# Optimization experiments

Measured on AMD Instinct MI355X. Metric: run time of the kernel, lower is better.

The kernel has to match this reference:

```python
import jax, jax.numpy as jnp
import numpy as np

IN_FEATURES = 4096
OUT_FEATURES = 4096
Q_MAX = 127.0  # int8 activation range
EPS = 1e-10


def setup_inputs() -> dict:
    key = jax.random.key(0)
    k1, k2, k3 = jax.random.split(key, 3)
    x = jax.random.normal(k1, (4, 2048, IN_FEATURES), dtype=jnp.float32)
    # Ternary weight in {-1, 0, +1} (the unpacked content of w_packed from pack_tl1).
    w_raw = jax.random.normal(k2, (OUT_FEATURES, IN_FEATURES), dtype=jnp.float32)
    scale = jnp.mean(jnp.abs(w_raw))  # quantize_ternary: scale = |w|.mean()
    w_t = jnp.clip(jnp.round(w_raw / (scale + EPS)), -1.0, 1.0)
    bias = jax.random.normal(k3, (OUT_FEATURES,), dtype=jnp.float32)
    return {"x": x, "w_t": w_t, "w_scale": scale, "bias": bias}


def reference(x, w_t, w_scale, bias):
    """TernaryLinear forward: per-row int8 activation quant, ternary matmul
    with int32 accumulation, scale dequant, bias add.

    x: [..., in], w_t: [out, in] in {-1,0,+1}, w_scale: scalar, bias: [out].
    """
    lead = x.shape[:-1]
    x2 = x.reshape(-1, IN_FEATURES)  # [T, in]
    # Per-row absmax int8 quantization of activations.
    absmax = jnp.max(jnp.abs(x2), axis=-1, keepdims=True)  # [T, 1]
    act_scale = jnp.maximum(absmax, EPS) / Q_MAX
    xq = jnp.clip(jnp.round(x2 / act_scale), -Q_MAX, Q_MAX)  # int-valued [T, in]
    # int32 accumulation (exact in int32; values bounded by 127 * 4096).
    acc = jnp.matmul(xq.astype(jnp.int32), w_t.astype(jnp.int32).T)  # [T, out]
    # Dequantize: y ~= (x @ w_t.T) * w_scale, then bias.
    y = acc.astype(jnp.float32) * act_scale * w_scale + bias
    return y.reshape(*lead, OUT_FEATURES)
```

## Files before the change

### kernel.cpp

```cpp
#include <hip/hip_runtime.h>
#include <stdint.h>

#define T_ROWS 8192
#define IN_F 4096
#define OUT_F 4096

using i32x4 = __attribute__((ext_vector_type(4))) int;

#define GLOBAL_AS __attribute__((address_space(1)))
#define LDS_AS __attribute__((address_space(3)))

static __device__ __forceinline__ void load_lds16(const void* g, void* l) {
    __builtin_amdgcn_global_load_lds((const GLOBAL_AS uint32_t*)g,
                                     (LDS_AS uint32_t*)l, 16, 0, 0);
}

__global__ __launch_bounds__(256) void prep_kernel(const float* __restrict__ x,
                                                   int8_t* __restrict__ xq,
                                                   float* __restrict__ scales,
                                                   const float* __restrict__ w,
                                                   int8_t* __restrict__ w8) {
    if (blockIdx.x < T_ROWS) {
        const int row = blockIdx.x;
        const float* xr = x + (size_t)row * IN_F;
        const float4* xr4 = (const float4*)xr;

        float4 v[4];
        float amax = 0.0f;
#pragma unroll
        for (int i = 0; i < 4; ++i) {
            v[i] = xr4[threadIdx.x + 256 * i];
            amax = fmaxf(amax, fmaxf(fmaxf(fabsf(v[i].x), fabsf(v[i].y)),
                                     fmaxf(fabsf(v[i].z), fabsf(v[i].w))));
        }
#pragma unroll
        for (int off = 32; off; off >>= 1)
            amax = fmaxf(amax, __shfl_xor(amax, off, 64));
        __shared__ float smax[4];
        if ((threadIdx.x & 63) == 0) smax[threadIdx.x >> 6] = amax;
        __syncthreads();
        amax = fmaxf(fmaxf(smax[0], smax[1]), fmaxf(smax[2], smax[3]));

        const float act_scale = fmaxf(amax, 1e-10f) / 127.0f;
        if (threadIdx.x == 0) scales[row] = act_scale;

        int* xqr = (int*)(xq + (size_t)row * IN_F);
#pragma unroll
        for (int i = 0; i < 4; ++i) {
            int q0 = (int)fminf(fmaxf(rintf(v[i].x / act_scale), -127.0f), 127.0f);
            int q1 = (int)fminf(fmaxf(rintf(v[i].y / act_scale), -127.0f), 127.0f);
            int q2 = (int)fminf(fmaxf(rintf(v[i].z / act_scale), -127.0f), 127.0f);
            int q3 = (int)fminf(fmaxf(rintf(v[i].w / act_scale), -127.0f), 127.0f);
            int packed = (q0 & 0xff) | ((q1 & 0xff) << 8) | ((q2 & 0xff) << 16) | (q3 << 24);
            xqr[threadIdx.x + 256 * i] = packed;
        }
    } else {
        const float4* w4 = (const float4*)w;
        int* o4 = (int*)w8;
        size_t base = (size_t)(blockIdx.x - T_ROWS) * 1024 + threadIdx.x;
#pragma unroll
        for (int i = 0; i < 4; ++i) {
            size_t idx = base + 256 * i;
            float4 v = w4[idx];
            int q0 = (int)v.x, q1 = (int)v.y, q2 = (int)v.z, q3 = (int)v.w;
            o4[idx] = (q0 & 0xff) | ((q1 & 0xff) << 8) | ((q2 & 0xff) << 16) | (q3 << 24);
        }
    }
}

__global__ __launch_bounds__(512, 2) void gemm_kernel(const int8_t* __restrict__ xq,
                                                      const int8_t* __restrict__ w8,
                                                      const float* __restrict__ scales,
                                                      const float* __restrict__ bias,
                                                      const float* __restrict__ wscale_p,
                                                      float* __restrict__ out) {
    __shared__ __align__(16) int8_t As[2 * 256 * 128];
    __shared__ __align__(16) int8_t Bs[2 * 256 * 128];

    const int tid = threadIdx.x;
    const int lane = tid & 63;
    const int w = tid >> 6;
    const int wr = w >> 2;
    const int wc = w & 3;
    const int l16 = lane & 15;
    const int lq = lane >> 4;

    int bid = blockIdx.x;
    bid = (bid & 7) * 64 + (bid >> 3);
    const int brow = (bid >> 4) * 256;
    const int bcol = (bid & 15) * 256;

    const int lrow = lane >> 3;
    const int lslot = (lane & 7) ^ lrow;
    const int8_t* srcA = xq + (size_t)(brow + lrow) * IN_F + lslot * 16;
    const int8_t* srcB = w8 + (size_t)(bcol + lrow) * IN_F + lslot * 16;

    const int sA = l16 & 7;
    const int8_t* pA0 = As + (wr * 16 + l16) * 128 + ((lq ^ sA) << 4);
    const int8_t* pA1 = As + (wr * 16 + l16) * 128 + (((lq ^ sA) ^ 4) << 4);
    const int8_t* pB0 = Bs + (wc * 16 + l16) * 128 + ((lq ^ sA) << 4);
    const int8_t* pB1 = Bs + (wc * 16 + l16) * 128 + (((lq ^ sA) ^ 4) << 4);

#define STAGE(LDSA, SRC, BUF, H, KT) do {                                          \
    load_lds16((SRC) + (size_t)((H) * 128 + w * 8) * IN_F + (KT) * 128,            \
               (void*)((LDSA) + (BUF) * 32768 + ((H) * 16 + w) * 1024));           \
    load_lds16((SRC) + (size_t)((H) * 128 + (w + 8) * 8) * IN_F + (KT) * 128,      \
               (void*)((LDSA) + (BUF) * 32768 + ((H) * 16 + w + 8) * 1024));       \
} while (0)

#define READ_A(BUF, MH)                                                            \
    _Pragma("unroll") for (int m = 0; m < 4; ++m) {                                \
        ra[m][0] = *(const i32x4*)(pA0 + (BUF) * 32768 + ((MH) * 4 + m) * 4096);   \
        ra[m][1] = *(const i32x4*)(pA1 + (BUF) * 32768 + ((MH) * 4 + m) * 4096);   \
    }

#define READ_B(BUF, NH, RB)                                                        \
    _Pragma("unroll") for (int n = 0; n < 2; ++n) {                                \
        RB[n][0] = *(const i32x4*)(pB0 + (BUF) * 32768 + ((NH) * 2 + n) * 8192);   \
        RB[n][1] = *(const i32x4*)(pB1 + (BUF) * 32768 + ((NH) * 2 + n) * 8192);   \
    }

#define PHASE(READS, STAGE_STMT, MH, NH, RB, VM_STMT) do {                         \
    READS;                                                                         \
    STAGE_STMT;                                                                    \
    __builtin_amdgcn_s_setprio(1);                                                 \
    _Pragma("unroll") for (int m = 0; m < 4; ++m)                                  \
    _Pragma("unroll") for (int n = 0; n < 2; ++n) {                                \
        acc[(MH) * 4 + m][(NH) * 2 + n] = __builtin_amdgcn_mfma_i32_16x16x64_i8(   \
            ra[m][0], RB[n][0], acc[(MH) * 4 + m][(NH) * 2 + n], 0, 0, 0);         \
        acc[(MH) * 4 + m][(NH) * 2 + n] = __builtin_amdgcn_mfma_i32_16x16x64_i8(   \
            ra[m][1], RB[n][1], acc[(MH) * 4 + m][(NH) * 2 + n], 0, 0, 0);         \
    }                                                                              \
    __builtin_amdgcn_s_setprio(0);                                                 \
    VM_STMT;                                                                       \
    __builtin_amdgcn_s_barrier();                                                  \
    asm volatile("" ::: "memory");                                                 \
} while (0)

    i32x4 acc[8][4] = {};
    i32x4 ra[4][2], rb0[2][2], rb1[2][2];

    STAGE(As, srcA, 0, 0, 0);
    STAGE(Bs, srcB, 0, 0, 0);
    STAGE(Bs, srcB, 0, 1, 0);
    STAGE(As, srcA, 0, 1, 0);
    STAGE(As, srcA, 1, 0, 1);
    STAGE(Bs, srcB, 1, 0, 1);
    STAGE(Bs, srcB, 1, 1, 1);
    asm volatile("s_waitcnt vmcnt(6)" ::: "memory");
    __builtin_amdgcn_s_barrier();
    asm volatile("" ::: "memory");

    for (int t = 0; t < 16; ++t) {
        const int k1 = 2 * t + 1;
        const int k2 = (2 * t + 2) & 31;
        const int k3 = (2 * t + 3) & 31;
        PHASE(READ_B(0, 0, rb0); READ_A(0, 0), STAGE(As, srcA, 1, 1, k1), 0, 0, rb0, );
        PHASE(READ_B(0, 1, rb1),               STAGE(As, srcA, 0, 0, k2), 0, 1, rb1, );
        PHASE(READ_A(0, 1),                    STAGE(Bs, srcB, 0, 0, k2), 1, 1, rb1, );
        PHASE(,                                STAGE(Bs, srcB, 0, 1, k2), 1, 0, rb0,
              asm volatile("s_waitcnt vmcnt(6)" ::: "memory"));
        PHASE(READ_B(1, 0, rb0); READ_A(1, 0), STAGE(As, srcA, 0, 1, k2), 0, 0, rb0, );
        PHASE(READ_B(1, 1, rb1),               STAGE(As, srcA, 1, 0, k3), 0, 1, rb1, );
        PHASE(READ_A(1, 1),                    STAGE(Bs, srcB, 1, 0, k3), 1, 1, rb1, );
        PHASE(,                                STAGE(Bs, srcB, 1, 1, k3), 1, 0, rb0,
              asm volatile("s_waitcnt vmcnt(6)" ::: "memory"));
    }

    const float ws = wscale_p[0];
#pragma unroll
    for (int m = 0; m < 8; ++m) {
        const int row0 = brow + m * 32 + wr * 16 + lq * 4;
#pragma unroll
        for (int j = 0; j < 4; ++j) {
            const int row = row0 + j;
            const float sc = scales[row] * ws;
#pragma unroll
            for (int n = 0; n < 4; ++n) {
                const int col = bcol + n * 64 + wc * 16 + l16;
                out[(size_t)row * OUT_F + col] = (float)acc[m][n][j] * sc + bias[col];
            }
        }
    }
#undef STAGE
#undef READ_A
#undef READ_B
#undef PHASE
}

extern "C" void kernel_launch(void* const* d_in, const int* in_sizes, int n_in,
                              void* d_out, int out_size, void* d_ws, size_t ws_size,
                              hipStream_t stream) {
    const float* x       = (const float*)d_in[0];
    const float* w_t     = (const float*)d_in[1];
    const float* w_scale = (const float*)d_in[2];
    const float* bias    = (const float*)d_in[3];
    float* out = (float*)d_out;

    int8_t* xq     = (int8_t*)d_ws;
    float*  scales = (float*)((char*)d_ws + (size_t)T_ROWS * IN_F);
    int8_t* w8     = (int8_t*)((char*)d_ws + (size_t)T_ROWS * IN_F + T_ROWS * sizeof(float));

    prep_kernel<<<T_ROWS + (OUT_F * IN_F) / (16 * 256), 256, 0, stream>>>(
        x, xq, scales, w_t, w8);

    gemm_kernel<<<(T_ROWS / 256) * (OUT_F / 256), 512, 0, stream>>>(
        xq, w8, scales, bias, w_scale, out);
}
```

Measured before the change: 178.9 us.

## Switch GEMM to 32x32x32 int8 MFMA with contiguous per-wave tiles and new pipeline

Replaces the 16x16x64 int8 MFMA tiling with 32x32x32 MFMA, so each wave now owns a contiguous 128x64 output block with 4x2 accumulator tiles of 16 ints. LDS fragment reads are reorganized per K-slice with double-buffered register fragments, and the staging/barrier schedule is rewritten to full vmcnt(0) waits per half-iteration. The larger MFMA shape cuts LDS read traffic per flop and instruction count. The stricter vmcnt(0) waits may expose more global-load latency than the previous partial-wait pipeline.

```diff
diff --git a/kernel.cpp b/kernel.cpp
--- a/kernel.cpp
+++ b/kernel.cpp
@@ -6,6 +6,7 @@
 #define OUT_F 4096
 
 using i32x4 = __attribute__((ext_vector_type(4))) int;
+using i32x16 = __attribute__((ext_vector_type(16))) int;
 
 #define GLOBAL_AS __attribute__((address_space(1)))
 #define LDS_AS __attribute__((address_space(3)))
@@ -82,8 +83,9 @@
     const int w = tid >> 6;
     const int wr = w >> 2;
     const int wc = w & 3;
-    const int l16 = lane & 15;
-    const int lq = lane >> 4;
+    const int l31 = lane & 31;
+    const int lh = lane >> 5;
+    const int le = lane & 7;
 
     int bid = blockIdx.x;
     bid = (bid & 7) * 64 + (bid >> 3);
@@ -95,11 +97,10 @@
     const int8_t* srcA = xq + (size_t)(brow + lrow) * IN_F + lslot * 16;
     const int8_t* srcB = w8 + (size_t)(bcol + lrow) * IN_F + lslot * 16;
 
-    const int sA = l16 & 7;
-    const int8_t* pA0 = As + (wr * 16 + l16) * 128 + ((lq ^ sA) << 4);
-    const int8_t* pA1 = As + (wr * 16 + l16) * 128 + (((lq ^ sA) ^ 4) << 4);
-    const int8_t* pB0 = Bs + (wc * 16 + l16) * 128 + ((lq ^ sA) << 4);
-    const int8_t* pB1 = Bs + (wc * 16 + l16) * 128 + (((lq ^ sA) ^ 4) << 4);
+    const int aBase = (wr * 128 + l31) * 128;
+    const int bBase = (wc * 64 + l31) * 128;
+    const int slo[4] = { ((0 + lh) ^ le) << 4, ((2 + lh) ^ le) << 4,
+                         ((4 + lh) ^ le) << 4, ((6 + lh) ^ le) << 4 };
 
 #define STAGE(LDSA, SRC, BUF, H, KT) do {                                          \
     load_lds16((SRC) + (size_t)((H) * 128 + w * 8) * IN_F + (KT) * 128,            \
@@ -108,84 +109,94 @@
                (void*)((LDSA) + (BUF) * 32768 + ((H) * 16 + w + 8) * 1024));       \
 } while (0)
 
-#define READ_A(BUF, MH)                                                            \
-    _Pragma("unroll") for (int m = 0; m < 4; ++m) {                                \
-        ra[m][0] = *(const i32x4*)(pA0 + (BUF) * 32768 + ((MH) * 4 + m) * 4096);   \
-        ra[m][1] = *(const i32x4*)(pA1 + (BUF) * 32768 + ((MH) * 4 + m) * 4096);   \
-    }
-
-#define READ_B(BUF, NH, RB)                                                        \
-    _Pragma("unroll") for (int n = 0; n < 2; ++n) {                                \
-        RB[n][0] = *(const i32x4*)(pB0 + (BUF) * 32768 + ((NH) * 2 + n) * 8192);   \
-        RB[n][1] = *(const i32x4*)(pB1 + (BUF) * 32768 + ((NH) * 2 + n) * 8192);   \
-    }
-
-#define PHASE(READS, STAGE_STMT, MH, NH, RB, VM_STMT) do {                         \
-    READS;                                                                         \
-    STAGE_STMT;                                                                    \
+#define PF(FA, FB, BUF, KS) do {                                                   \
+    _Pragma("unroll") for (int mi = 0; mi < 4; ++mi)                               \
+        FA[mi] = *(const i32x4*)(As + (BUF) * 32768 + aBase + mi * 4096 + slo[KS]);\
+    _Pragma("unroll") for (int ni = 0; ni < 2; ++ni)                               \
+        FB[ni] = *(const i32x4*)(Bs + (BUF) * 32768 + bBase + ni * 4096 + slo[KS]);\
+} while (0)
+
+#define MFMA8(FA, FB) do {                                                         \
     __builtin_amdgcn_s_setprio(1);                                                 \
-    _Pragma("unroll") for (int m = 0; m < 4; ++m)                                  \
-    _Pragma("unroll") for (int n = 0; n < 2; ++n) {                                \
-        acc[(MH) * 4 + m][(NH) * 2 + n] = __builtin_amdgcn_mfma_i32_16x16x64_i8(   \
-            ra[m][0], RB[n][0], acc[(MH) * 4 + m][(NH) * 2 + n], 0, 0, 0);         \
-        acc[(MH) * 4 + m][(NH) * 2 + n] = __builtin_amdgcn_mfma_i32_16x16x64_i8(   \
-            ra[m][1], RB[n][1], acc[(MH) * 4 + m][(NH) * 2 + n], 0, 0, 0);         \
-    }                                                                              \
+    _Pragma("unroll") for (int mi = 0; mi < 4; ++mi)                               \
+    _Pragma("unroll") for (int ni = 0; ni < 2; ++ni)                               \
+        acc[mi][ni] = __builtin_amdgcn_mfma_i32_32x32x32_i8(FA[mi], FB[ni],        \
+                                                            acc[mi][ni], 0, 0, 0); \
     __builtin_amdgcn_s_setprio(0);                                                 \
-    VM_STMT;                                                                       \
-    __builtin_amdgcn_s_barrier();                                                  \
-    asm volatile("" ::: "memory");                                                 \
 } while (0)
 
-    i32x4 acc[8][4] = {};
-    i32x4 ra[4][2], rb0[2][2], rb1[2][2];
+#define BARFENCE do { __builtin_amdgcn_s_barrier(); asm volatile("" ::: "memory"); } while (0)
+#define VM0 asm volatile("s_waitcnt vmcnt(0)" ::: "memory")
+
+    i32x16 acc[4][2] = {};
+    i32x4 a0[4], b0[2], a1[4], b1[2];
 
     STAGE(As, srcA, 0, 0, 0);
+    STAGE(As, srcA, 0, 1, 0);
     STAGE(Bs, srcB, 0, 0, 0);
     STAGE(Bs, srcB, 0, 1, 0);
-    STAGE(As, srcA, 0, 1, 0);
-    STAGE(As, srcA, 1, 0, 1);
-    STAGE(Bs, srcB, 1, 0, 1);
-    STAGE(Bs, srcB, 1, 1, 1);
-    asm volatile("s_waitcnt vmcnt(6)" ::: "memory");
-    __builtin_amdgcn_s_barrier();
-    asm volatile("" ::: "memory");
+    VM0;
+    BARFENCE;
+    PF(a0, b0, 0, 0);
 
     for (int t = 0; t < 16; ++t) {
-        const int k1 = 2 * t + 1;
+        const int k1 = (2 * t + 1) & 31;
         const int k2 = (2 * t + 2) & 31;
-        const int k3 = (2 * t + 3) & 31;
-        PHASE(READ_B(0, 0, rb0); READ_A(0, 0), STAGE(As, srcA, 1, 1, k1), 0, 0, rb0, );
-        PHASE(READ_B(0, 1, rb1),               STAGE(As, srcA, 0, 0, k2), 0, 1, rb1, );
-        PHASE(READ_A(0, 1),                    STAGE(Bs, srcB, 0, 0, k2), 1, 1, rb1, );
-        PHASE(,                                STAGE(Bs, srcB, 0, 1, k2), 1, 0, rb0,
-              asm volatile("s_waitcnt vmcnt(6)" ::: "memory"));
-        PHASE(READ_B(1, 0, rb0); READ_A(1, 0), STAGE(As, srcA, 0, 1, k2), 0, 0, rb0, );
-        PHASE(READ_B(1, 1, rb1),               STAGE(As, srcA, 1, 0, k3), 0, 1, rb1, );
-        PHASE(READ_A(1, 1),                    STAGE(Bs, srcB, 1, 0, k3), 1, 1, rb1, );
-        PHASE(,                                STAGE(Bs, srcB, 1, 1, k3), 1, 0, rb0,
-              asm volatile("s_waitcnt vmcnt(6)" ::: "memory"));
+        PF(a1, b1, 0, 1);
+        STAGE(As, srcA, 1, 0, k1);
+        STAGE(As, srcA, 1, 1, k1);
+        STAGE(Bs, srcB, 1, 0, k1);
+        MFMA8(a0, b0);
+        PF(a0, b0, 0, 2);
+        STAGE(Bs, srcB, 1, 1, k1);
+        MFMA8(a1, b1);
+        PF(a1, b1, 0, 3);
+        MFMA8(a0, b0);
+        VM0;
+        BARFENCE;
+        PF(a0, b0, 1, 0);
+        MFMA8(a1, b1);
+        BARFENCE;
+        PF(a1, b1, 1, 1);
+        STAGE(As, srcA, 0, 0, k2);
+        STAGE(As, srcA, 0, 1, k2);
+        STAGE(Bs, srcB, 0, 0, k2);
+        MFMA8(a0, b0);
+        PF(a0, b0, 1, 2);
+        STAGE(Bs, srcB, 0, 1, k2);
+        MFMA8(a1, b1);
+        PF(a1, b1, 1, 3);
+        MFMA8(a0, b0);
+        VM0;
+        BARFENCE;
+        PF(a0, b0, 0, 0);
+        MFMA8(a1, b1);
+        BARFENCE;
     }
 
     const float ws = wscale_p[0];
 #pragma unroll
-    for (int m = 0; m < 8; ++m) {
-        const int row0 = brow + m * 32 + wr * 16 + lq * 4;
-#pragma unroll
-        for (int j = 0; j < 4; ++j) {
-            const int row = row0 + j;
-            const float sc = scales[row] * ws;
-#pragma unroll
-            for (int n = 0; n < 4; ++n) {
-                const int col = bcol + n * 64 + wc * 16 + l16;
-                out[(size_t)row * OUT_F + col] = (float)acc[m][n][j] * sc + bias[col];
+    for (int mi = 0; mi < 4; ++mi) {
+#pragma unroll
+        for (int q = 0; q < 4; ++q) {
+#pragma unroll
+            for (int r = 0; r < 4; ++r) {
+                const int row = brow + wr * 128 + mi * 32 + q * 8 + r + 4 * lh;
+                const float sc = scales[row] * ws;
+#pragma unroll
+                for (int ni = 0; ni < 2; ++ni) {
+                    const int col = bcol + wc * 64 + ni * 32 + l31;
+                    out[(size_t)row * OUT_F + col] =
+                        (float)acc[mi][ni][q * 4 + r] * sc + bias[col];
+                }
             }
         }
     }
 #undef STAGE
-#undef READ_A
-#undef READ_B
-#undef PHASE
+#undef PF
+#undef MFMA8
+#undef BARFENCE
+#undef VM0
 }
 
 extern "C" void kernel_launch(void* const* d_in, const int* in_sizes, int n_in,
```

Measured after the change: 192.5 us. +7.6%, slower.

## Load B tiles directly from global into registers, bypassing LDS

Applied to the files above, without the earlier changes.

Removes the shared-memory staging buffer for the weight operand. Each wave now loads its own B fragments straight from global memory into registers, while only A goes through LDS with double buffering. The block-to-tile mapping also changes so each XCD owns a pair of column tiles, which is meant to improve L2 reuse of weights. This halves LDS use and LDS traffic, but each B fragment is now fetched by multiple waves from global/L2 with less latency hiding, since only one tile of register prefetch is kept.

```diff
diff --git a/kernel.cpp b/kernel.cpp
--- a/kernel.cpp
+++ b/kernel.cpp
@@ -75,7 +75,6 @@
                                                       const float* __restrict__ wscale_p,
                                                       float* __restrict__ out) {
     __shared__ __align__(16) int8_t As[2 * 256 * 128];
-    __shared__ __align__(16) int8_t Bs[2 * 256 * 128];
 
     const int tid = threadIdx.x;
     const int lane = tid & 63;
@@ -85,27 +84,31 @@
     const int l16 = lane & 15;
     const int lq = lane >> 4;
 
-    int bid = blockIdx.x;
-    bid = (bid & 7) * 64 + (bid >> 3);
-    const int brow = (bid >> 4) * 256;
-    const int bcol = (bid & 15) * 256;
+    const int orig = blockIdx.x;
+    const int xcd = orig & 7;
+    const int j = orig >> 3;
+    const int brow = (j >> 1) * 256;
+    const int bcol = (xcd * 2 + (j & 1)) * 256;
 
     const int lrow = lane >> 3;
     const int lslot = (lane & 7) ^ lrow;
     const int8_t* srcA = xq + (size_t)(brow + lrow) * IN_F + lslot * 16;
-    const int8_t* srcB = w8 + (size_t)(bcol + lrow) * IN_F + lslot * 16;
 
     const int sA = l16 & 7;
     const int8_t* pA0 = As + (wr * 16 + l16) * 128 + ((lq ^ sA) << 4);
     const int8_t* pA1 = As + (wr * 16 + l16) * 128 + (((lq ^ sA) ^ 4) << 4);
-    const int8_t* pB0 = Bs + (wc * 16 + l16) * 128 + ((lq ^ sA) << 4);
-    const int8_t* pB1 = Bs + (wc * 16 + l16) * 128 + (((lq ^ sA) ^ 4) << 4);
-
-#define STAGE(LDSA, SRC, BUF, H, KT) do {                                          \
-    load_lds16((SRC) + (size_t)((H) * 128 + w * 8) * IN_F + (KT) * 128,            \
-               (void*)((LDSA) + (BUF) * 32768 + ((H) * 16 + w) * 1024));           \
-    load_lds16((SRC) + (size_t)((H) * 128 + (w + 8) * 8) * IN_F + (KT) * 128,      \
-               (void*)((LDSA) + (BUF) * 32768 + ((H) * 16 + w + 8) * 1024));       \
+
+    const int8_t* pBsrc = w8 + (size_t)(bcol + wc * 16 + l16) * IN_F + lq * 16;
+
+#define STAGE_A(BUF, KT) do {                                                      \
+    load_lds16(srcA + (size_t)(0 * 128 + w * 8) * IN_F + (KT) * 128,               \
+               (void*)(As + (BUF) * 32768 + (0 * 16 + w) * 1024));                 \
+    load_lds16(srcA + (size_t)(0 * 128 + (w + 8) * 8) * IN_F + (KT) * 128,         \
+               (void*)(As + (BUF) * 32768 + (0 * 16 + w + 8) * 1024));             \
+    load_lds16(srcA + (size_t)(1 * 128 + w * 8) * IN_F + (KT) * 128,               \
+               (void*)(As + (BUF) * 32768 + (1 * 16 + w) * 1024));                 \
+    load_lds16(srcA + (size_t)(1 * 128 + (w + 8) * 8) * IN_F + (KT) * 128,         \
+               (void*)(As + (BUF) * 32768 + (1 * 16 + w + 8) * 1024));             \
 } while (0)
 
 #define READ_A(BUF, MH)                                                            \
@@ -114,57 +117,61 @@
         ra[m][1] = *(const i32x4*)(pA1 + (BUF) * 32768 + ((MH) * 4 + m) * 4096);   \
     }
 
-#define READ_B(BUF, NH, RB)                                                        \
-    _Pragma("unroll") for (int n = 0; n < 2; ++n) {                                \
-        RB[n][0] = *(const i32x4*)(pB0 + (BUF) * 32768 + ((NH) * 2 + n) * 8192);   \
-        RB[n][1] = *(const i32x4*)(pB1 + (BUF) * 32768 + ((NH) * 2 + n) * 8192);   \
-    }
-
-#define PHASE(READS, STAGE_STMT, MH, NH, RB, VM_STMT) do {                         \
-    READS;                                                                         \
-    STAGE_STMT;                                                                    \
+#define LOAD_BN(DST, NBASE, KT)                                                    \
+    _Pragma("unroll") for (int jj = 0; jj < 2; ++jj)                               \
+    _Pragma("unroll") for (int ks = 0; ks < 2; ++ks)                               \
+        DST[jj][ks] = *(const i32x4*)(pBsrc + (size_t)(((NBASE) + jj) * 64) * IN_F \
+                                      + (KT) * 128 + ks * 64);
+
+#define MFMA16(MH, NH, BREG) do {                                                  \
     __builtin_amdgcn_s_setprio(1);                                                 \
     _Pragma("unroll") for (int m = 0; m < 4; ++m)                                  \
     _Pragma("unroll") for (int n = 0; n < 2; ++n) {                                \
         acc[(MH) * 4 + m][(NH) * 2 + n] = __builtin_amdgcn_mfma_i32_16x16x64_i8(   \
-            ra[m][0], RB[n][0], acc[(MH) * 4 + m][(NH) * 2 + n], 0, 0, 0);         \
+            ra[m][0], BREG[n][0], acc[(MH) * 4 + m][(NH) * 2 + n], 0, 0, 0);       \
         acc[(MH) * 4 + m][(NH) * 2 + n] = __builtin_amdgcn_mfma_i32_16x16x64_i8(   \
-            ra[m][1], RB[n][1], acc[(MH) * 4 + m][(NH) * 2 + n], 0, 0, 0);         \
+            ra[m][1], BREG[n][1], acc[(MH) * 4 + m][(NH) * 2 + n], 0, 0, 0);       \
     }                                                                              \
     __builtin_amdgcn_s_setprio(0);                                                 \
-    VM_STMT;                                                                       \
+} while (0)
+
+#define FENCE asm volatile("" ::: "memory")
+
+#define KTILE(BUF, KT, KN) do {                                                    \
+                                                                           \
+    READ_A(BUF, 0);                                                                \
+    LOAD_BN(bn1, 2, KT);                                                           \
+    MFMA16(0, 0, bn0);                                                             \
+                                                                           \
+    MFMA16(0, 1, bn1);                                                             \
+                                                                           \
+    READ_A(BUF, 1);                                                                \
+    STAGE_A((BUF) ^ 1, KN);                                                        \
+    FENCE;                                                                         \
+    MFMA16(1, 1, bn1);                                                             \
+                                                                           \
+    MFMA16(1, 0, bn0);                                                             \
+    LOAD_BN(bn0, 0, KN);                                                           \
+    asm volatile("s_waitcnt vmcnt(4)" ::: "memory");                               \
     __builtin_amdgcn_s_barrier();                                                  \
-    asm volatile("" ::: "memory");                                                 \
+    FENCE;                                                                         \
 } while (0)
 
     i32x4 acc[8][4] = {};
-    i32x4 ra[4][2], rb0[2][2], rb1[2][2];
-
-    STAGE(As, srcA, 0, 0, 0);
-    STAGE(Bs, srcB, 0, 0, 0);
-    STAGE(Bs, srcB, 0, 1, 0);
-    STAGE(As, srcA, 0, 1, 0);
-    STAGE(As, srcA, 1, 0, 1);
-    STAGE(Bs, srcB, 1, 0, 1);
-    STAGE(Bs, srcB, 1, 1, 1);
-    asm volatile("s_waitcnt vmcnt(6)" ::: "memory");
+    i32x4 ra[4][2], bn0[2][2], bn1[2][2];
+
+    STAGE_A(0, 0);
+    LOAD_BN(bn0, 0, 0);
+    asm volatile("s_waitcnt vmcnt(0)" ::: "memory");
     __builtin_amdgcn_s_barrier();
-    asm volatile("" ::: "memory");
+    FENCE;
 
     for (int t = 0; t < 16; ++t) {
+        const int k0 = 2 * t;
         const int k1 = 2 * t + 1;
         const int k2 = (2 * t + 2) & 31;
-        const int k3 = (2 * t + 3) & 31;
-        PHASE(READ_B(0, 0, rb0); READ_A(0, 0), STAGE(As, srcA, 1, 1, k1), 0, 0, rb0, );
-        PHASE(READ_B(0, 1, rb1),               STAGE(As, srcA, 0, 0, k2), 0, 1, rb1, );
-        PHASE(READ_A(0, 1),                    STAGE(Bs, srcB, 0, 0, k2), 1, 1, rb1, );
-        PHASE(,                                STAGE(Bs, srcB, 0, 1, k2), 1, 0, rb0,
-              asm volatile("s_waitcnt vmcnt(6)" ::: "memory"));
-        PHASE(READ_B(1, 0, rb0); READ_A(1, 0), STAGE(As, srcA, 0, 1, k2), 0, 0, rb0, );
-        PHASE(READ_B(1, 1, rb1),               STAGE(As, srcA, 1, 0, k3), 0, 1, rb1, );
-        PHASE(READ_A(1, 1),                    STAGE(Bs, srcB, 1, 0, k3), 1, 1, rb1, );
-        PHASE(,                                STAGE(Bs, srcB, 1, 1, k3), 1, 0, rb0,
-              asm volatile("s_waitcnt vmcnt(6)" ::: "memory"));
+        KTILE(0, k0, k1);
+        KTILE(1, k1, k2);
     }
 
     const float ws = wscale_p[0];
@@ -172,20 +179,22 @@
     for (int m = 0; m < 8; ++m) {
         const int row0 = brow + m * 32 + wr * 16 + lq * 4;
 #pragma unroll
-        for (int j = 0; j < 4; ++j) {
-            const int row = row0 + j;
+        for (int jj = 0; jj < 4; ++jj) {
+            const int row = row0 + jj;
             const float sc = scales[row] * ws;
 #pragma unroll
             for (int n = 0; n < 4; ++n) {
                 const int col = bcol + n * 64 + wc * 16 + l16;
-                out[(size_t)row * OUT_F + col] = (float)acc[m][n][j] * sc + bias[col];
+                out[(size_t)row * OUT_F + col] = (float)acc[m][n][jj] * sc + bias[col];
             }
         }
     }
-#undef STAGE
+#undef STAGE_A
 #undef READ_A
-#undef READ_B
-#undef PHASE
+#undef LOAD_BN
+#undef MFMA16
+#undef FENCE
+#undef KTILE
 }
 
 extern "C" void kernel_launch(void* const* d_in, const int* in_sizes, int n_in,
```

Result: slower. 224.0 us (+25.2%).
